# Performance work log

Hardware: AMD Instinct MI355X
Metric: run time of the kernel (lower is better)

The kernel has to match this reference:

```python
import jax, jax.numpy as jnp
import numpy as np

N_QUBITS = 4  # kernel 2x2 -> 4 pixels -> 4 qubits -> 4 PauliZ outputs
KH, KW = 2, 2
STRIDE = 2
OUT_CHANNELS = 4


def _cnot(state, c, t):
    # state: [P, 2,2,2,2]; qubit q lives on axis q+1
    ca, ta = c + 1, t + 1
    s0 = jax.lax.index_in_dim(state, 0, ca, keepdims=True)
    s1 = jnp.flip(jax.lax.index_in_dim(state, 1, ca, keepdims=True), axis=ta)
    return jnp.concatenate([s0, s1], axis=ca)


def _ry(state, theta_q, q):
    c, s = jnp.cos(theta_q / 2), jnp.sin(theta_q / 2)
    M = jnp.stack([jnp.stack([c, -s]), jnp.stack([s, c])])  # [2,2] real RY
    out = jnp.tensordot(M, state, axes=([1], [q + 1]))
    return jnp.moveaxis(out, 0, q + 1)


def _qnode(angles, theta):
    # angles: [P, 4] patch pixels used as RY embedding angles
    c, s = jnp.cos(angles / 2), jnp.sin(angles / 2)
    # product state |psi> = RY(a0)|0> x RY(a1)|0> x RY(a2)|0> x RY(a3)|0>
    state = jnp.einsum('pa,pb,pc,pd->pabcd',
                       jnp.stack([c[:, 0], s[:, 0]], -1),
                       jnp.stack([c[:, 1], s[:, 1]], -1),
                       jnp.stack([c[:, 2], s[:, 2]], -1),
                       jnp.stack([c[:, 3], s[:, 3]], -1))
    for q in range(N_QUBITS):            # entangling CNOT ring
        state = _cnot(state, q, (q + 1) % N_QUBITS)
    for q in range(N_QUBITS):            # trainable RY layer
        state = _ry(state, theta[q], q)
    p = state * state                    # real amplitudes -> probabilities
    outs = []
    for q in range(N_QUBITS):            # <Z_q> expectation values
        axes = tuple(a for a in range(1, N_QUBITS + 1) if a != q + 1)
        m = jnp.sum(p, axis=axes)        # [P, 2]
        outs.append(m[:, 0] - m[:, 1])
    return jnp.stack(outs, axis=-1)      # [P, 4]


def _quanv(xc, theta, out_per):
    # xc: [B, 1, H, W]; stride == kernel so unfold == blocked reshape
    B, _, H, W = xc.shape
    Ho, Wo = (H - KH) // STRIDE + 1, (W - KW) // STRIDE + 1
    # unfold ordering: patch pixels row-major (di*KW+dj), patches row-major over (Ho,Wo)
    patches = xc.reshape(B, Ho, KH, Wo, KW).transpose(0, 1, 3, 2, 4).reshape(B, Ho * Wo, KH * KW)
    # torch.stack over unbound patch dim puts L (patches) outermost: [L, B, 4]
    patches = patches.transpose(1, 0, 2).reshape(-1, KH * KW)  # [L*B, 4]
    vals = _qnode(patches, theta)                              # [L*B, 4]
    # faithful to the original raw .view of the contiguous [L, B, 4] buffer
    return vals.reshape(B, out_per, Ho, Wo)


def reference(x, theta):
    B, C, H, W = x.shape
    out_per = OUT_CHANNELS // C
    outs = [_quanv(x[:, c:c + 1], theta, out_per) for c in range(C)]
    return jnp.concatenate(outs, axis=1)


def setup_inputs() -> dict:
    key = jax.random.key(0)
    k1, k2 = jax.random.split(key)
    x = jax.random.normal(k1, (32, 1, 512, 512), dtype=jnp.float32)
    theta = jax.random.normal(k2, (4,), dtype=jnp.float32)
    return {"x": x, "theta": theta}
```

## Files before the change

kernel.cpp:

```cpp
#include <hip/hip_runtime.h>

#define BATCH 32
#define HH 512
#define WW 512
#define HO 256
#define WO 256
#define LTOT (HO * WO)

#define INV_4PI 0.07957747154594767f

__global__ __launch_bounds__(256) void quanv_kernel(const float* __restrict__ x,
                                                    const float* __restrict__ theta,
                                                    float* __restrict__ out) {
    __shared__ float4 lds[2048];

    const int tid   = threadIdx.x;
    const int l0    = blockIdx.x * 64;
    const int irow  = l0 >> 8;
    const int j0    = l0 & 255;
    const int lpair = tid & 31;
    const int b0    = tid >> 5;

    float ct[4], st[4];
#pragma unroll
    for (int q = 0; q < 4; ++q) {
        const float r = theta[q] * INV_4PI;
        st[q] = __builtin_amdgcn_sinf(r);
        ct[q] = __builtin_amdgcn_cosf(r);
    }

    const int col  = 2 * (j0 + 2 * lpair);
    const int off0 = (2 * irow) * WW + col;
    const int off1 = off0 + WW;

#pragma unroll
    for (int pp = 0; pp < 4; ++pp) {
        const int b = b0 + pp * 8;
        const float* xb = x + (size_t)b * (HH * WW);
        const float4 r0 = *(const float4*)(xb + off0);
        const float4 r1 = *(const float4*)(xb + off1);

#pragma unroll
        for (int c = 0; c < 2; ++c) {
            const float aa[4] = {c ? r0.z : r0.x, c ? r0.w : r0.y,
                                 c ? r1.z : r1.x, c ? r1.w : r1.y};
            float pc[4], ps[4];
#pragma unroll
            for (int k = 0; k < 4; ++k) {
                const float r = aa[k] * INV_4PI;
                ps[k] = __builtin_amdgcn_sinf(r);
                pc[k] = __builtin_amdgcn_cosf(r);
            }

            float amp[16];
#pragma unroll
            for (int s = 0; s < 16; ++s) {
                float v = ((s & 8) ? ps[0] : pc[0]);
                v *= ((s & 4) ? ps[1] : pc[1]);
                v *= ((s & 2) ? ps[2] : pc[2]);
                v *= ((s & 1) ? ps[3] : pc[3]);
                amp[s] = v;
            }

#pragma unroll
            for (int g = 0; g < 4; ++g) {
                const int cb = 8 >> g;
                const int tb = 8 >> ((g + 1) & 3);
#pragma unroll
                for (int s = 0; s < 16; ++s) {
                    if ((s & cb) && !(s & tb)) {
                        float tmp = amp[s];
                        amp[s] = amp[s ^ tb];
                        amp[s ^ tb] = tmp;
                    }
                }
            }

#pragma unroll
            for (int q = 0; q < 4; ++q) {
                const int qb = 8 >> q;
                const float cc = ct[q], sv = st[q];
#pragma unroll
                for (int s = 0; s < 16; ++s) {
                    if (!(s & qb)) {
                        float v0 = amp[s], v1 = amp[s | qb];
                        amp[s]      = cc * v0 - sv * v1;
                        amp[s | qb] = sv * v0 + cc * v1;
                    }
                }
            }

            float z0 = 0.f, z1 = 0.f, z2 = 0.f, z3 = 0.f;
#pragma unroll
            for (int s = 0; s < 16; ++s) {
                float p = amp[s] * amp[s];
                z0 += (s & 8) ? -p : p;
                z1 += (s & 4) ? -p : p;
                z2 += (s & 2) ? -p : p;
                z3 += (s & 1) ? -p : p;
            }

            const int lsub = 2 * lpair + c;
            lds[lsub * 32 + (b ^ (lsub & 31))] = make_float4(z0, z1, z2, z3);
        }
    }

    __syncthreads();

    float4* out4 = (float4*)out + (size_t)l0 * 32;
#pragma unroll
    for (int k = 0; k < 8; ++k) {
        const int idx = k * 256 + tid;
        const int ls = idx >> 5, bb = idx & 31;
        out4[idx] = lds[ls * 32 + (bb ^ (ls & 31))];
    }
}

extern "C" void kernel_launch(void* const* d_in, const int* in_sizes, int n_in,
                              void* d_out, int out_size, void* d_ws, size_t ws_size,
                              hipStream_t stream) {
    const float* x     = (const float*)d_in[0];
    const float* theta = (const float*)d_in[1];
    float* out         = (float*)d_out;

    const int blocks = LTOT / 64;
    quanv_kernel<<<blocks, 256, 0, stream>>>(x, theta, out);
}
```

Before: 91.58 us.

## Replace statevector simulation with closed-form Pauli-Z expectations and halve block tile

Result: faster. 80.92 us (-11.6%).

```diff
diff --git a/kernel.cpp b/kernel.cpp
--- a/kernel.cpp
+++ b/kernel.cpp
@@ -1,30 +1,29 @@
 #include <hip/hip_runtime.h>
 
-#define BATCH 32
 #define HH 512
 #define WW 512
 #define HO 256
 #define WO 256
 #define LTOT (HO * WO)
 
-#define INV_4PI 0.07957747154594767f
+#define INV_2PI 0.15915494309189535f
 
 __global__ __launch_bounds__(256) void quanv_kernel(const float* __restrict__ x,
                                                     const float* __restrict__ theta,
                                                     float* __restrict__ out) {
-    __shared__ float4 lds[2048];
+    __shared__ float4 lds[1024];
 
     const int tid   = threadIdx.x;
-    const int l0    = blockIdx.x * 64;
+    const int l0    = blockIdx.x * 32;
     const int irow  = l0 >> 8;
     const int j0    = l0 & 255;
-    const int lpair = tid & 31;
-    const int b0    = tid >> 5;
+    const int lpair = tid & 15;
+    const int b0    = tid >> 4;
 
     float ct[4], st[4];
 #pragma unroll
     for (int q = 0; q < 4; ++q) {
-        const float r = theta[q] * INV_4PI;
+        const float r = theta[q] * INV_2PI;
         st[q] = __builtin_amdgcn_sinf(r);
         ct[q] = __builtin_amdgcn_cosf(r);
     }
@@ -33,72 +32,41 @@
     const int off0 = (2 * irow) * WW + col;
     const int off1 = off0 + WW;
 
+    const float* xb0 = x + (size_t)b0 * (HH * WW);
+    const float* xb1 = x + (size_t)(b0 + 16) * (HH * WW);
+    const float4 r0a = *(const float4*)(xb0 + off0);
+    const float4 r1a = *(const float4*)(xb0 + off1);
+    const float4 r0b = *(const float4*)(xb1 + off0);
+    const float4 r1b = *(const float4*)(xb1 + off1);
+
 #pragma unroll
-    for (int pp = 0; pp < 4; ++pp) {
-        const int b = b0 + pp * 8;
-        const float* xb = x + (size_t)b * (HH * WW);
-        const float4 r0 = *(const float4*)(xb + off0);
-        const float4 r1 = *(const float4*)(xb + off1);
-
+    for (int w = 0; w < 2; ++w) {
+        const int b = b0 + 16 * w;
+        const float4 r0 = w ? r0b : r0a;
+        const float4 r1 = w ? r1b : r1a;
 #pragma unroll
         for (int c = 0; c < 2; ++c) {
             const float aa[4] = {c ? r0.z : r0.x, c ? r0.w : r0.y,
                                  c ? r1.z : r1.x, c ? r1.w : r1.y};
-            float pc[4], ps[4];
+            float ca[4], sa[4];
 #pragma unroll
             for (int k = 0; k < 4; ++k) {
-                const float r = aa[k] * INV_4PI;
-                ps[k] = __builtin_amdgcn_sinf(r);
-                pc[k] = __builtin_amdgcn_cosf(r);
+                const float r = aa[k] * INV_2PI;
+                sa[k] = __builtin_amdgcn_sinf(r);
+                ca[k] = __builtin_amdgcn_cosf(r);
             }
-
-            float amp[16];
-#pragma unroll
-            for (int s = 0; s < 16; ++s) {
-                float v = ((s & 8) ? ps[0] : pc[0]);
-                v *= ((s & 4) ? ps[1] : pc[1]);
-                v *= ((s & 2) ? ps[2] : pc[2]);
-                v *= ((s & 1) ? ps[3] : pc[3]);
-                amp[s] = v;
-            }
-
-#pragma unroll
-            for (int g = 0; g < 4; ++g) {
-                const int cb = 8 >> g;
-                const int tb = 8 >> ((g + 1) & 3);
-#pragma unroll
-                for (int s = 0; s < 16; ++s) {
-                    if ((s & cb) && !(s & tb)) {
-                        float tmp = amp[s];
-                        amp[s] = amp[s ^ tb];
-                        amp[s ^ tb] = tmp;
-                    }
-                }
-            }
-
-#pragma unroll
-            for (int q = 0; q < 4; ++q) {
-                const int qb = 8 >> q;
-                const float cc = ct[q], sv = st[q];
-#pragma unroll
-                for (int s = 0; s < 16; ++s) {
-                    if (!(s & qb)) {
-                        float v0 = amp[s], v1 = amp[s | qb];
-                        amp[s]      = cc * v0 - sv * v1;
-                        amp[s | qb] = sv * v0 + cc * v1;
-                    }
-                }
-            }
-
-            float z0 = 0.f, z1 = 0.f, z2 = 0.f, z3 = 0.f;
-#pragma unroll
-            for (int s = 0; s < 16; ++s) {
-                float p = amp[s] * amp[s];
-                z0 += (s & 8) ? -p : p;
-                z1 += (s & 4) ? -p : p;
-                z2 += (s & 2) ? -p : p;
-                z3 += (s & 1) ? -p : p;
-            }
+            const float A1 = ca[0] * ca[1];
+            const float A2 = A1 * ca[2];
+            const float A3 = A2 * ca[3];
+            const float A0 = (ca[1] * ca[2]) * ca[3];
+            const float B0 = sa[0] * sa[1];
+            const float B1 = sa[1] * sa[2];
+            const float B2 = sa[2] * sa[3];
+            const float B3 = B0 * sa[3];
+            const float z0 = ct[0] * A0 - st[0] * B0;
+            const float z1 = ct[1] * A1 - st[1] * B1;
+            const float z2 = ct[2] * A2 - st[2] * B2;
+            const float z3 = ct[3] * A3 - st[3] * B3;
 
             const int lsub = 2 * lpair + c;
             lds[lsub * 32 + (b ^ (lsub & 31))] = make_float4(z0, z1, z2, z3);
@@ -109,7 +77,7 @@
 
     float4* out4 = (float4*)out + (size_t)l0 * 32;
 #pragma unroll
-    for (int k = 0; k < 8; ++k) {
+    for (int k = 0; k < 4; ++k) {
         const int idx = k * 256 + tid;
         const int ls = idx >> 5, bb = idx & 31;
         out4[idx] = lds[ls * 32 + (bb ^ (ls & 31))];
@@ -123,6 +91,6 @@
     const float* theta = (const float*)d_in[1];
     float* out         = (float*)d_out;
 
-    const int blocks = LTOT / 64;
+    const int blocks = LTOT / 32;
     quanv_kernel<<<blocks, 256, 0, stream>>>(x, theta, out);
 }
```
